# Performance work log

Hardware: AMD Instinct MI355X
Metric: run time of the kernel (lower is better)

## Reference

```python
import jax, jax.numpy as jnp
import numpy as np


def setup_inputs() -> dict:
    key = jax.random.key(0)
    x = jax.random.normal(key, (32, 64, 128, 128), dtype=jnp.float32)
    return {"x": x}


def reference(x) -> jnp.ndarray:
    # Inverse wavelet transform: x is [4B, C, H, W] -> [B, C, 2H, 2W]
    B4, C, H, W = x.shape
    B = B4 // 4
    x1 = x[0 * B:1 * B] * 0.5
    x2 = x[1 * B:2 * B] * 0.5
    x3 = x[2 * B:3 * B] * 0.5
    x4 = x[3 * B:4 * B] * 0.5
    # Values by (row parity p, col parity q) of output pixel (2i+p, 2j+q)
    e00 = x1 - x2 - x3 + x4  # even row, even col
    e01 = x1 + x2 - x3 - x4  # even row, odd col
    e10 = x1 - x2 + x3 - x4  # odd row, even col
    e11 = x1 + x2 + x3 + x4  # odd row, odd col
    top = jnp.stack([e00, e01], axis=-1)     # [B, C, H, W, 2]
    bot = jnp.stack([e10, e11], axis=-1)     # [B, C, H, W, 2]
    h = jnp.stack([top, bot], axis=3)        # [B, C, H, 2, W, 2]
    return h.reshape(B, C, 2 * H, 2 * W)
```

## Files before the change

kernel.cpp:

```cpp
#include <hip/hip_runtime.h>


typedef float f2 __attribute__((ext_vector_type(2)));
typedef float f4 __attribute__((ext_vector_type(4)));

constexpr int H = 128, W = 128;
constexpr int HW = H * W;
constexpr int OUT_ROW = 2 * W;
constexpr int OUT_PLANE = 4 * HW;

__global__ __launch_bounds__(256) void iwt_kernel(const float* __restrict__ x,
                                                  float* __restrict__ out,
                                                  int quarter,
                                                  int total_vec)
{
    int tid = blockIdx.x * blockDim.x + threadIdx.x;
    if (tid >= total_vec) return;

    int jv2 = tid & 63;
    int i   = (tid >> 6) & (H - 1);
    int cb  = tid >> 13;

    int in_off = cb * HW + i * W + (jv2 << 1);

    const f2 a1 = *reinterpret_cast<const f2*>(x + in_off);
    const f2 a2 = *reinterpret_cast<const f2*>(x + in_off + quarter);
    const f2 a3 = *reinterpret_cast<const f2*>(x + in_off + 2 * quarter);
    const f2 a4 = *reinterpret_cast<const f2*>(x + in_off + 3 * quarter);

    float s1 = a1[0] * 0.5f, s2 = a2[0] * 0.5f, s3 = a3[0] * 0.5f, s4 = a4[0] * 0.5f;
    float e00a = s1 - s2 - s3 + s4;
    float e01a = s1 + s2 - s3 - s4;
    float e10a = s1 - s2 + s3 - s4;
    float e11a = s1 + s2 + s3 + s4;
    float t1 = a1[1] * 0.5f, t2 = a2[1] * 0.5f, t3 = a3[1] * 0.5f, t4 = a4[1] * 0.5f;
    float e00b = t1 - t2 - t3 + t4;
    float e01b = t1 + t2 - t3 - t4;
    float e10b = t1 - t2 + t3 - t4;
    float e11b = t1 + t2 + t3 + t4;

    int out_top = cb * OUT_PLANE + (2 * i) * OUT_ROW + (jv2 << 2);
    int out_bot = out_top + OUT_ROW;

    f4 vt = {e00a, e01a, e00b, e01b};
    f4 vb = {e10a, e11a, e10b, e11b};

    __builtin_nontemporal_store(vt, reinterpret_cast<f4*>(out + out_top));
    __builtin_nontemporal_store(vb, reinterpret_cast<f4*>(out + out_bot));
}

extern "C" void kernel_launch(void* const* d_in, const int* in_sizes, int n_in,
                              void* d_out, int out_size, void* d_ws, size_t ws_size,
                              hipStream_t stream) {
    const float* x = (const float*)d_in[0];
    float* out = (float*)d_out;

    const int quarter   = in_sizes[0] / 4;
    const int total_vec = out_size / 8;
    const int block = 256;
    const int grid  = (total_vec + block - 1) / block;

    iwt_kernel<<<grid, block, 0, stream>>>(x, out, quarter, total_vec);
}
```

Baseline: 226.6 us.

## Widen input loads to 16 bytes via LDS exchange and loop row pairs per block

Each wave now loads one quarter's pair of input rows with 16-byte vector loads and stages them in shared memory. Each wave then reads the four quarters' values back from shared memory and writes one full output row. Each block walks four row pairs, which shrinks the grid to 8192 blocks. The goal is wider, more coalesced global reads and fewer blocks, at the cost of two __syncthreads per iteration plus LDS traffic.

```diff
diff --git a/kernel.cpp b/kernel.cpp
--- a/kernel.cpp
+++ b/kernel.cpp
@@ -8,45 +8,64 @@
 constexpr int HW = H * W;
 constexpr int OUT_ROW = 2 * W;
 constexpr int OUT_PLANE = 4 * HW;
+constexpr int PAIRS = 4;
 
 __global__ __launch_bounds__(256) void iwt_kernel(const float* __restrict__ x,
                                                   float* __restrict__ out,
-                                                  int quarter,
-                                                  int total_vec)
+                                                  int quarter)
 {
-    int tid = blockIdx.x * blockDim.x + threadIdx.x;
-    if (tid >= total_vec) return;
+    __shared__ f4 lds[4 * 64];
 
-    int jv2 = tid & 63;
-    int i   = (tid >> 6) & (H - 1);
-    int cb  = tid >> 13;
+    const int t    = threadIdx.x;
+    const int wq   = t >> 6;
+    const int lane = t & 63;
 
-    int in_off = cb * HW + i * W + (jv2 << 1);
+    const int cb  = blockIdx.x >> 4;
+    const int ipg = blockIdx.x & 15;
 
-    const f2 a1 = *reinterpret_cast<const f2*>(x + in_off);
-    const f2 a2 = *reinterpret_cast<const f2*>(x + in_off + quarter);
-    const f2 a3 = *reinterpret_cast<const f2*>(x + in_off + 2 * quarter);
-    const f2 a4 = *reinterpret_cast<const f2*>(x + in_off + 3 * quarter);
+    const float* xq = x + wq * quarter + cb * HW + (lane << 2);
 
-    float s1 = a1[0] * 0.5f, s2 = a2[0] * 0.5f, s3 = a3[0] * 0.5f, s4 = a4[0] * 0.5f;
-    float e00a = s1 - s2 - s3 + s4;
-    float e01a = s1 + s2 - s3 - s4;
-    float e10a = s1 - s2 + s3 - s4;
-    float e11a = s1 + s2 + s3 + s4;
-    float t1 = a1[1] * 0.5f, t2 = a2[1] * 0.5f, t3 = a3[1] * 0.5f, t4 = a4[1] * 0.5f;
-    float e00b = t1 - t2 - t3 + t4;
-    float e01b = t1 + t2 - t3 - t4;
-    float e10b = t1 - t2 + t3 - t4;
-    float e11b = t1 + t2 + t3 + t4;
+    const int ii_rel = wq >> 1;
+    const int p      = wq & 1;
+    const int u      = (ii_rel << 5) + (lane >> 1);
+    const int sub    = (lane & 1) << 1;
+    const float* lbase = reinterpret_cast<const float*>(lds) + u * 4 + sub;
+    float* obase = out + cb * OUT_PLANE + wq * OUT_ROW + (lane << 2);
 
-    int out_top = cb * OUT_PLANE + (2 * i) * OUT_ROW + (jv2 << 2);
-    int out_bot = out_top + OUT_ROW;
+#pragma unroll
+    for (int it = 0; it < PAIRS; ++it) {
+        const int ip = ipg * PAIRS + it;
+        const int i0 = ip << 1;
 
-    f4 vt = {e00a, e01a, e00b, e01b};
-    f4 vb = {e10a, e11a, e10b, e11b};
+        f4 v = *reinterpret_cast<const f4*>(xq + i0 * W);
 
-    __builtin_nontemporal_store(vt, reinterpret_cast<f4*>(out + out_top));
-    __builtin_nontemporal_store(vb, reinterpret_cast<f4*>(out + out_bot));
+        __syncthreads();
+        lds[(wq << 6) + lane] = v;
+        __syncthreads();
+
+        f2 v1 = *reinterpret_cast<const f2*>(lbase + 0 * 256);
+        f2 v2 = *reinterpret_cast<const f2*>(lbase + 1 * 256);
+        f2 v3 = *reinterpret_cast<const f2*>(lbase + 2 * 256);
+        f2 v4 = *reinterpret_cast<const f2*>(lbase + 3 * 256);
+
+        float a1 = v1[0] * 0.5f, a2 = v2[0] * 0.5f, a3 = v3[0] * 0.5f, a4 = v4[0] * 0.5f;
+        float b1 = v1[1] * 0.5f, b2 = v2[1] * 0.5f, b3 = v3[1] * 0.5f, b4 = v4[1] * 0.5f;
+
+        f4 o;
+        if (p == 0) {
+            o[0] = a1 - a2 - a3 + a4;
+            o[1] = a1 + a2 - a3 - a4;
+            o[2] = b1 - b2 - b3 + b4;
+            o[3] = b1 + b2 - b3 - b4;
+        } else {
+            o[0] = a1 - a2 + a3 - a4;
+            o[1] = a1 + a2 + a3 + a4;
+            o[2] = b1 - b2 + b3 - b4;
+            o[3] = b1 + b2 + b3 + b4;
+        }
+
+        __builtin_nontemporal_store(o, reinterpret_cast<f4*>(obase + (i0 << 1) * OUT_ROW));
+    }
 }
 
 extern "C" void kernel_launch(void* const* d_in, const int* in_sizes, int n_in,
@@ -55,10 +74,10 @@
     const float* x = (const float*)d_in[0];
     float* out = (float*)d_out;
 
-    const int quarter   = in_sizes[0] / 4;
-    const int total_vec = out_size / 8;
-    const int block = 256;
-    const int grid  = (total_vec + block - 1) / block;
+    const int quarter = in_sizes[0] / 4;
+    const int n_cb    = quarter / HW;
+    const int grid    = n_cb * (H / 2 / PAIRS);
+    const int block   = 256;
 
-    iwt_kernel<<<grid, block, 0, stream>>>(x, out, quarter, total_vec);
+    iwt_kernel<<<grid, block, 0, stream>>>(x, out, quarter);
 }
```

After: 234.4 us. +3.4%, slower.
